# Performance work log

Hardware: AMD Instinct MI355X
Metric: run time of the kernel (lower is better)

The kernel has to match this reference:

```python
import jax, jax.numpy as jnp
import numpy as np

HID, S, SD = 4096, 64, 256
EPS = 1e-5
SCALE = SD ** -0.5


def layer_norm(x, w, b):
    mu = jnp.mean(x, axis=-1, keepdims=True)
    var = jnp.mean(jnp.square(x - mu), axis=-1, keepdims=True)
    return (x - mu) * jax.lax.rsqrt(var + EPS) * w + b


def setup_inputs() -> dict:
    key = jax.random.key(0)
    ks = jax.random.split(key, 9)
    B, T = 4, 4096
    w = lambda k, i, o: jax.random.normal(k, (i, o), jnp.float32) * 0.02
    return {
        "segment_hidden": jax.random.normal(ks[0], (B, T, HID), jnp.float32),
        "slot_embeddings": jax.random.normal(ks[1], (S, HID), jnp.float32) * 0.02,
        "Wq": w(ks[2], HID, SD),
        "Wk": w(ks[3], HID, SD),
        "Wv": w(ks[4], HID, SD),
        "Wo": w(ks[5], SD, HID),
        "Wrq": w(ks[6], HID, SD),
        "Wro": w(ks[7], SD, HID),
        "gate_bias": jnp.full((S,), 2.0, jnp.float32),
        "slot_norm_w": jnp.ones((HID,), jnp.float32),
        "slot_norm_b": jnp.zeros((HID,), jnp.float32),
        "recon_norm_w": jnp.ones((HID,), jnp.float32),
        "recon_norm_b": jnp.zeros((HID,), jnp.float32),
    }


def reference(segment_hidden, slot_embeddings, Wq, Wk, Wv, Wo, Wrq, Wro,
              gate_bias, slot_norm_w, slot_norm_b, recon_norm_w, recon_norm_b):
    B = segment_hidden.shape[0]
    slots = jnp.broadcast_to(slot_embeddings[None], (B, S, HID))

    # 1) slot attention: slots attend to segment
    q = slots @ Wq                      # [B,S,sd]
    k = segment_hidden @ Wk             # [B,T,sd]
    v = segment_hidden @ Wv             # [B,T,sd]
    attn = jax.nn.softmax(jnp.einsum('bsd,btd->bst', q, k) * SCALE, axis=-1)
    out = jnp.einsum('bst,btd->bsd', attn, v) @ Wo
    updated_slots = layer_norm(slots + out, slot_norm_w, slot_norm_b)  # [B,S,D]

    # 2) reconstruction: segment attends to updated slots
    rq = segment_hidden @ Wrq           # [B,T,sd]
    rk = updated_slots @ Wk             # [B,S,sd]
    rv = updated_slots @ Wv             # [B,S,sd]
    rattn = jax.nn.softmax(jnp.einsum('btd,bsd->bts', rq, rk) * SCALE, axis=-1)
    rout = jnp.einsum('bts,bsd->btd', rattn, rv) @ Wro
    rout = layer_norm(rout, recon_norm_w, recon_norm_b)
    scalar_gate = jax.nn.sigmoid(jnp.mean(gate_bias))[None, None, None]  # [1,1,1]
    reconstruction = scalar_gate * rout

    # 3) MSE reconstruction loss
    recon_loss = jnp.mean(jnp.square(reconstruction - segment_hidden))
    return updated_slots, recon_loss, scalar_gate
```

## Files before the change

kernel.cpp:

```cpp
#include <hip/hip_runtime.h>
#include <hip/hip_bf16.h>


#define DEVI __device__ __forceinline__

typedef __attribute__((ext_vector_type(4))) float f32x4;
typedef __attribute__((ext_vector_type(8))) __bf16 bf16x8;

DEVI float bf2f(unsigned short u) {
    unsigned int x = ((unsigned int)u) << 16;
    return __uint_as_float(x);
}
DEVI unsigned short f2bf(float f) {
    unsigned int u = __float_as_uint(f);
    unsigned int r = (u + 0x7FFFu + ((u >> 16) & 1u)) >> 16;
    return (unsigned short)r;
}

DEVI void gl_lds16(const void* g, void* l) {
    __builtin_amdgcn_global_load_lds(
        (const __attribute__((address_space(1))) void*)g,
        (__attribute__((address_space(3))) void*)l, 16, 0, 0);
}

__global__ __launch_bounds__(256) void k_cvt_bf16(const float* __restrict__ in,
                                                  unsigned short* __restrict__ out,
                                                  long n) {
    long i = ((long)blockIdx.x * blockDim.x + threadIdx.x) * 4;
    long stride = (long)gridDim.x * blockDim.x * 4;
    for (long j = i; j < n; j += stride) {
        float4 v = *(const float4*)(in + j);
        ushort4 o;
        o.x = f2bf(v.x); o.y = f2bf(v.y); o.z = f2bf(v.z); o.w = f2bf(v.w);
        *(ushort4*)(out + j) = o;
    }
}

__global__ __launch_bounds__(256) void k_transpose_f2b(const float* __restrict__ in, int ldin, long long sIn,
                                                       unsigned short* __restrict__ out, int ldout, long long sOut) {
    __shared__ float tile[32][33];
    in += (long long)blockIdx.z * sIn;
    out += (long long)blockIdx.z * sOut;
    int c0 = blockIdx.x * 32, r0 = blockIdx.y * 32;
    int tx = threadIdx.x, ty = threadIdx.y;
#pragma unroll
    for (int i = 0; i < 4; i++)
        tile[ty + i * 8][tx] = in[(size_t)(r0 + ty + i * 8) * ldin + c0 + tx];
    __syncthreads();
#pragma unroll
    for (int i = 0; i < 4; i++)
        out[(size_t)(c0 + ty + i * 8) * ldout + r0 + tx] = f2bf(tile[tx][ty + i * 8]);
}

__global__ __launch_bounds__(256) void k_transpose_b2b(const unsigned short* __restrict__ in, int ldin, long long sIn,
                                                       unsigned short* __restrict__ out, int ldout, long long sOut) {
    __shared__ unsigned short tile[32][33];
    in += (long long)blockIdx.z * sIn;
    out += (long long)blockIdx.z * sOut;
    int c0 = blockIdx.x * 32, r0 = blockIdx.y * 32;
    int tx = threadIdx.x, ty = threadIdx.y;
#pragma unroll
    for (int i = 0; i < 4; i++)
        tile[ty + i * 8][tx] = in[(size_t)(r0 + ty + i * 8) * ldin + c0 + tx];
    __syncthreads();
#pragma unroll
    for (int i = 0; i < 4; i++)
        out[(size_t)(c0 + ty + i * 8) * ldout + r0 + tx] = tile[tx][ty + i * 8];
}

template <int BM, int BN, int WR, int WC, int OMODE>
__global__ __launch_bounds__(256) void k_gemm(const unsigned short* __restrict__ A, int lda, long long sA,
                                              const unsigned short* __restrict__ B, int ldb, long long sB,
                                              void* __restrict__ Cv, int ldc, long long sC,
                                              int K, int ksplit, float alpha) {
    constexpr int NW = WR * WC;
    static_assert(NW == 4, "4 waves");
    __shared__ alignas(1024) unsigned short As[BM * 64];
    __shared__ alignas(1024) unsigned short Bs[BN * 64];
    const int tid = threadIdx.x;
    const int lane = tid & 63;
    const int wv = tid >> 6;
    const int batch = blockIdx.z / ksplit;
    const int ks = blockIdx.z - batch * ksplit;
    const unsigned short* Ab = A + (long long)batch * sA;
    const unsigned short* Bb = B + (long long)batch * sB;
    const int bm0 = blockIdx.x * BM;
    const int bn0 = blockIdx.y * BN;
    const int kchunk = K / ksplit;
    const int kt0 = (ks * kchunk) >> 6;
    const int kt1 = ((ks + 1) * kchunk) >> 6;

    constexpr int WTM = BM / WR, WTN = BN / WC;
    constexpr int FM = WTM / 16, FN = WTN / 16;
    const int wr = wv / WC, wc = wv % WC;

    f32x4 acc[FM][FN] = {};

    constexpr int CA = BM / 8, CB = BN / 8;
    constexpr int PW = (CA + CB) / NW;

    for (int kt = kt0; kt < kt1; ++kt) {
        const int k0 = kt << 6;
#pragma unroll
        for (int i = 0; i < PW; i++) {
            int c = wv * PW + i;
            if (c < CA) {
                int row = bm0 + c * 8 + (lane >> 3);
                gl_lds16(Ab + (size_t)row * lda + k0 + (lane & 7) * 8, (void*)(As + c * 512));
            } else {
                int cc = c - CA;
                int row = bn0 + cc * 8 + (lane >> 3);
                gl_lds16(Bb + (size_t)row * ldb + k0 + (lane & 7) * 8, (void*)(Bs + cc * 512));
            }
        }
        asm volatile("s_waitcnt vmcnt(0)" ::: "memory");
        __syncthreads();
#pragma unroll
        for (int kk = 0; kk < 2; ++kk) {
            const int kof = kk * 32 + (lane >> 4) * 8;
            bf16x8 af[FM], bfr[FN];
#pragma unroll
            for (int m = 0; m < FM; m++)
                af[m] = *(const bf16x8*)(As + (wr * WTM + m * 16 + (lane & 15)) * 64 + kof);
#pragma unroll
            for (int n = 0; n < FN; n++)
                bfr[n] = *(const bf16x8*)(Bs + (wc * WTN + n * 16 + (lane & 15)) * 64 + kof);
#pragma unroll
            for (int m = 0; m < FM; m++)
#pragma unroll
                for (int n = 0; n < FN; n++)
                    acc[m][n] = __builtin_amdgcn_mfma_f32_16x16x32_bf16(af[m], bfr[n], acc[m][n], 0, 0, 0);
        }
        __syncthreads();
    }

    float* Cf = (float*)Cv;
    unsigned short* Cb = (unsigned short*)Cv;
    const long long cbase = (long long)batch * sC;
#pragma unroll
    for (int m = 0; m < FM; m++) {
#pragma unroll
        for (int n = 0; n < FN; n++) {
            int gr0 = bm0 + wr * WTM + m * 16 + (lane >> 4) * 4;
            int gc = bn0 + wc * WTN + n * 16 + (lane & 15);
#pragma unroll
            for (int j = 0; j < 4; j++) {
                float v = alpha * acc[m][n][j];
                long long idx = cbase + (long long)(gr0 + j) * ldc + gc;
                if constexpr (OMODE == 0) Cf[idx] = v;
                else if constexpr (OMODE == 1) Cb[idx] = f2bf(v);
                else atomicAdd(Cf + idx, v);
            }
        }
    }
}

DEVI float block_sum(float v, float* sh) {
    int lane = threadIdx.x & 63, wv = threadIdx.x >> 6;
#pragma unroll
    for (int o = 32; o > 0; o >>= 1) v += __shfl_xor(v, o);
    __syncthreads();
    if (lane == 0) sh[wv] = v;
    __syncthreads();
    return sh[0] + sh[1] + sh[2] + sh[3];
}

__global__ __launch_bounds__(256) void k_softmax_T(const float* __restrict__ L,
                                                   unsigned short* __restrict__ out) {
    const size_t row = blockIdx.x;
    const float* x = L + row * 4096;
    float v[16];
    float mx = -1e30f;
#pragma unroll
    for (int i = 0; i < 4; i++) {
        float4 t = *(const float4*)(x + threadIdx.x * 4 + i * 1024);
        v[i * 4 + 0] = t.x; v[i * 4 + 1] = t.y; v[i * 4 + 2] = t.z; v[i * 4 + 3] = t.w;
        mx = fmaxf(fmaxf(fmaxf(mx, t.x), fmaxf(t.y, t.z)), t.w);
    }
    int lane = threadIdx.x & 63, wv = threadIdx.x >> 6;
#pragma unroll
    for (int o = 32; o > 0; o >>= 1) mx = fmaxf(mx, __shfl_xor(mx, o));
    __shared__ float smax[4], ssum[4];
    if (lane == 0) smax[wv] = mx;
    __syncthreads();
    mx = fmaxf(fmaxf(smax[0], smax[1]), fmaxf(smax[2], smax[3]));
    float sum = 0.f;
#pragma unroll
    for (int i = 0; i < 16; i++) {
        v[i] = __expf(v[i] - mx);
        sum += v[i];
    }
#pragma unroll
    for (int o = 32; o > 0; o >>= 1) sum += __shfl_xor(sum, o);
    if (lane == 0) ssum[wv] = sum;
    __syncthreads();
    float inv = 1.0f / (ssum[0] + ssum[1] + ssum[2] + ssum[3]);
    unsigned short* o = out + row * 4096;
#pragma unroll
    for (int i = 0; i < 4; i++) {
        ushort4 u;
        u.x = f2bf(v[i * 4 + 0] * inv); u.y = f2bf(v[i * 4 + 1] * inv);
        u.z = f2bf(v[i * 4 + 2] * inv); u.w = f2bf(v[i * 4 + 3] * inv);
        *(ushort4*)(o + threadIdx.x * 4 + i * 1024) = u;
    }
}

__global__ __launch_bounds__(256) void k_softmax_S(const float* __restrict__ L,
                                                   unsigned short* __restrict__ out) {
    size_t row = (size_t)blockIdx.x * 4 + (threadIdx.x >> 6);
    int lane = threadIdx.x & 63;
    float v = L[row * 64 + lane];
    float mx = v;
#pragma unroll
    for (int o = 32; o > 0; o >>= 1) mx = fmaxf(mx, __shfl_xor(mx, o));
    float e = __expf(v - mx), sum = e;
#pragma unroll
    for (int o = 32; o > 0; o >>= 1) sum += __shfl_xor(sum, o);
    out[row * 64 + lane] = f2bf(e / sum);
}

__global__ __launch_bounds__(256) void k_ln_slots(const float* __restrict__ slot_emb,
                                                  const float* __restrict__ out2,
                                                  const float* __restrict__ w,
                                                  const float* __restrict__ b,
                                                  float* __restrict__ us_out,
                                                  unsigned short* __restrict__ us_b) {
    __shared__ float sh[4];
    int row = blockIdx.x;
    int s = row & 63;
    const float* se_r = slot_emb + (size_t)s * 4096;
    const float* o2_r = out2 + (size_t)row * 4096;
    float x[16];
    float sum = 0.f;
#pragma unroll
    for (int i = 0; i < 4; i++) {
        int j0 = threadIdx.x * 4 + i * 1024;
        float4 a = *(const float4*)(se_r + j0);
        float4 c = *(const float4*)(o2_r + j0);
        x[i * 4 + 0] = a.x + c.x; x[i * 4 + 1] = a.y + c.y;
        x[i * 4 + 2] = a.z + c.z; x[i * 4 + 3] = a.w + c.w;
        sum += x[i * 4 + 0] + x[i * 4 + 1] + x[i * 4 + 2] + x[i * 4 + 3];
    }
    sum = block_sum(sum, sh);
    float mu = sum * (1.0f / 4096.0f);
    float s2 = 0.f;
#pragma unroll
    for (int i = 0; i < 16; i++) {
        float d = x[i] - mu;
        s2 += d * d;
    }
    s2 = block_sum(s2, sh);
    float rs = rsqrtf(s2 * (1.0f / 4096.0f) + 1e-5f);
#pragma unroll
    for (int i = 0; i < 4; i++) {
        int j0 = threadIdx.x * 4 + i * 1024;
        float4 wv4 = *(const float4*)(w + j0);
        float4 bv4 = *(const float4*)(b + j0);
        float4 y;
        y.x = (x[i * 4 + 0] - mu) * rs * wv4.x + bv4.x;
        y.y = (x[i * 4 + 1] - mu) * rs * wv4.y + bv4.y;
        y.z = (x[i * 4 + 2] - mu) * rs * wv4.z + bv4.z;
        y.w = (x[i * 4 + 3] - mu) * rs * wv4.w + bv4.w;
        *(float4*)(us_out + (size_t)row * 4096 + j0) = y;
        ushort4 u;
        u.x = f2bf(y.x); u.y = f2bf(y.y); u.z = f2bf(y.z); u.w = f2bf(y.w);
        *(ushort4*)(us_b + (size_t)row * 4096 + j0) = u;
    }
}

__global__ __launch_bounds__(256) void k_ln_loss(const unsigned short* __restrict__ rout_pre,
                                                 const float* __restrict__ seg,
                                                 const float* __restrict__ w,
                                                 const float* __restrict__ b,
                                                 const float* __restrict__ gate_s,
                                                 float* __restrict__ partials) {
    __shared__ float sh[4];
    size_t row = blockIdx.x;
    const unsigned short* xr = rout_pre + row * 4096;
    const float* sr = seg + row * 4096;
    float x[16];
    float sum = 0.f;
#pragma unroll
    for (int i = 0; i < 4; i++) {
        int j0 = threadIdx.x * 4 + i * 1024;
        ushort4 u = *(const ushort4*)(xr + j0);
        x[i * 4 + 0] = bf2f(u.x); x[i * 4 + 1] = bf2f(u.y);
        x[i * 4 + 2] = bf2f(u.z); x[i * 4 + 3] = bf2f(u.w);
        sum += x[i * 4 + 0] + x[i * 4 + 1] + x[i * 4 + 2] + x[i * 4 + 3];
    }
    sum = block_sum(sum, sh);
    float mu = sum * (1.0f / 4096.0f);
    float s2 = 0.f;
#pragma unroll
    for (int i = 0; i < 16; i++) {
        float d = x[i] - mu;
        s2 += d * d;
    }
    s2 = block_sum(s2, sh);
    float rs = rsqrtf(s2 * (1.0f / 4096.0f) + 1e-5f);
    float g = *gate_s;
    float ls = 0.f;
#pragma unroll
    for (int i = 0; i < 4; i++) {
        int j0 = threadIdx.x * 4 + i * 1024;
        float4 wv4 = *(const float4*)(w + j0);
        float4 bv4 = *(const float4*)(b + j0);
        float4 sv4 = *(const float4*)(sr + j0);
        float d0 = g * ((x[i * 4 + 0] - mu) * rs * wv4.x + bv4.x) - sv4.x;
        float d1 = g * ((x[i * 4 + 1] - mu) * rs * wv4.y + bv4.y) - sv4.y;
        float d2 = g * ((x[i * 4 + 2] - mu) * rs * wv4.z + bv4.z) - sv4.z;
        float d3 = g * ((x[i * 4 + 3] - mu) * rs * wv4.w + bv4.w) - sv4.w;
        ls += d0 * d0 + d1 * d1 + d2 * d2 + d3 * d3;
    }
    ls = block_sum(ls, sh);
    if (threadIdx.x == 0) partials[row] = ls;
}

__global__ void k_gate(const float* __restrict__ gb, float* __restrict__ gate_s) {
    int lane = threadIdx.x;
    float v = gb[lane];
#pragma unroll
    for (int o = 32; o > 0; o >>= 1) v += __shfl_xor(v, o);
    if (lane == 0) *gate_s = 1.0f / (1.0f + __expf(-(v * (1.0f / 64.0f))));
}

__global__ __launch_bounds__(1024) void k_loss_final(const float* __restrict__ partials,
                                                     const float* __restrict__ gate_s,
                                                     float* __restrict__ out) {
    __shared__ float sh[16];
    int t = threadIdx.x;
    float s = 0.f;
#pragma unroll
    for (int i = 0; i < 4; i++) {
        float4 v = *(const float4*)(partials + t * 16 + i * 4);
        s += v.x + v.y + v.z + v.w;
    }
#pragma unroll
    for (int o = 32; o > 0; o >>= 1) s += __shfl_xor(s, o);
    int lane = t & 63, wv = t >> 6;
    if (lane == 0) sh[wv] = s;
    __syncthreads();
    if (t == 0) {
        float tot = 0.f;
#pragma unroll
        for (int i = 0; i < 16; i++) tot += sh[i];
        out[1048576] = tot * (1.0f / 67108864.0f);
        out[1048577] = *gate_s;
    }
}

extern "C" void kernel_launch(void* const* d_in, const int* in_sizes, int n_in,
                              void* d_out, int out_size, void* d_ws, size_t ws_size,
                              hipStream_t stream) {
    const float* seg = (const float*)d_in[0];
    const float* se  = (const float*)d_in[1];
    const float* Wq  = (const float*)d_in[2];
    const float* Wk  = (const float*)d_in[3];
    const float* Wv  = (const float*)d_in[4];
    const float* Wo  = (const float*)d_in[5];
    const float* Wrq = (const float*)d_in[6];
    const float* Wro = (const float*)d_in[7];
    const float* gb  = (const float*)d_in[8];
    const float* snw = (const float*)d_in[9];
    const float* snb = (const float*)d_in[10];
    const float* rnw = (const float*)d_in[11];
    const float* rnb = (const float*)d_in[12];
    float* out = (float*)d_out;

    char* ws = (char*)d_ws;
    size_t off = 0;
    auto alloc = [&](size_t bytes) -> char* {
        char* p = ws + off;
        off += (bytes + 1023) & ~(size_t)1023;
        return p;
    };

    unsigned short* Xb    = (unsigned short*)alloc((size_t)16384 * 4096 * 2);
    unsigned short* KVQ   = (unsigned short*)alloc((size_t)16384 * 768 * 2);
    unsigned short* Wt    = (unsigned short*)alloc((size_t)1024 * 4096 * 2);
    unsigned short* Wot   = (unsigned short*)alloc((size_t)4096 * 256 * 2);
    unsigned short* Wrot  = (unsigned short*)alloc((size_t)4096 * 256 * 2);
    unsigned short* seb   = (unsigned short*)alloc((size_t)64 * 4096 * 2);
    float*          qf    = (float*)alloc((size_t)64 * 256 * 4);
    unsigned short* qb    = (unsigned short*)alloc((size_t)64 * 256 * 2);
    float*          L1    = (float*)alloc((size_t)4 * 64 * 4096 * 4);
    unsigned short* attn  = (unsigned short*)alloc((size_t)4 * 64 * 4096 * 2);
    unsigned short* Vt    = (unsigned short*)alloc((size_t)4 * 256 * 4096 * 2);
    float*          out1f = (float*)alloc((size_t)4 * 64 * 256 * 4);
    unsigned short* out1b = (unsigned short*)alloc((size_t)4 * 64 * 256 * 2);
    float*          out2  = (float*)alloc((size_t)256 * 4096 * 4);
    unsigned short* usb   = (unsigned short*)alloc((size_t)256 * 4096 * 2);
    float*          rkvf  = (float*)alloc((size_t)256 * 512 * 4);
    unsigned short* rkvb  = (unsigned short*)alloc((size_t)256 * 512 * 2);
    unsigned short* rvt   = (unsigned short*)alloc((size_t)4 * 256 * 64 * 2);
    unsigned short* rattn = (unsigned short*)alloc((size_t)4 * 4096 * 64 * 2);
    float*          gate_s = (float*)alloc(64);
    float*          partials = (float*)alloc((size_t)16384 * 4);
    unsigned short* routp = Xb;
    float*          L2    = L1;
    unsigned short* rmid  = Vt;

    hipMemsetAsync(out1f, 0, (size_t)4 * 64 * 256 * 4, stream);
    hipMemsetAsync(rkvf, 0, (size_t)256 * 512 * 4, stream);
    hipMemsetAsync(qf, 0, (size_t)64 * 256 * 4, stream);

    dim3 tb(32, 8);
    k_transpose_f2b<<<dim3(8, 128, 1), tb, 0, stream>>>(Wk, 256, 0, Wt, 4096, 0);
    k_transpose_f2b<<<dim3(8, 128, 1), tb, 0, stream>>>(Wv, 256, 0, Wt + (size_t)256 * 4096, 4096, 0);
    k_transpose_f2b<<<dim3(8, 128, 1), tb, 0, stream>>>(Wrq, 256, 0, Wt + (size_t)512 * 4096, 4096, 0);
    k_transpose_f2b<<<dim3(8, 128, 1), tb, 0, stream>>>(Wq, 256, 0, Wt + (size_t)768 * 4096, 4096, 0);
    k_transpose_f2b<<<dim3(128, 8, 1), tb, 0, stream>>>(Wo, 4096, 0, Wot, 256, 0);
    k_transpose_f2b<<<dim3(128, 8, 1), tb, 0, stream>>>(Wro, 4096, 0, Wrot, 256, 0);

    k_cvt_bf16<<<4096, 256, 0, stream>>>(seg, Xb, (long)67108864);
    k_cvt_bf16<<<256, 256, 0, stream>>>(se, seb, (long)262144);
    k_gate<<<1, 64, 0, stream>>>(gb, gate_s);

    k_gemm<64, 128, 1, 4, 2><<<dim3(1, 2, 16), 256, 0, stream>>>(
        seb, 4096, 0, Wt + (size_t)768 * 4096, 4096, 0, qf, 256, 0, 4096, 16, 1.0f);
    k_cvt_bf16<<<16, 256, 0, stream>>>(qf, qb, (long)16384);

    k_gemm<128, 128, 2, 2, 1><<<dim3(128, 6, 1), 256, 0, stream>>>(
        Xb, 4096, 0, Wt, 4096, 0, KVQ, 768, 0, 4096, 1, 1.0f);

    k_gemm<64, 128, 1, 4, 0><<<dim3(1, 32, 4), 256, 0, stream>>>(
        qb, 256, 0, KVQ, 768, 4096LL * 768, L1, 4096, 64LL * 4096, 256, 1, 0.0625f);
    k_softmax_T<<<256, 256, 0, stream>>>(L1, attn);

    k_transpose_b2b<<<dim3(8, 128, 4), tb, 0, stream>>>(KVQ + 256, 768, 4096LL * 768, Vt, 4096, 256LL * 4096);

    k_gemm<64, 128, 1, 4, 2><<<dim3(1, 2, 64), 256, 0, stream>>>(
        attn, 4096, 64LL * 4096, Vt, 4096, 256LL * 4096, out1f, 256, 64LL * 256, 4096, 16, 1.0f);
    k_cvt_bf16<<<64, 256, 0, stream>>>(out1f, out1b, (long)65536);

    k_gemm<64, 128, 1, 4, 0><<<dim3(4, 32, 1), 256, 0, stream>>>(
        out1b, 256, 0, Wot, 256, 0, out2, 4096, 0, 256, 1, 1.0f);

    k_ln_slots<<<256, 256, 0, stream>>>(se, out2, snw, snb, out, usb);

    k_gemm<64, 128, 1, 4, 2><<<dim3(4, 4, 16), 256, 0, stream>>>(
        usb, 4096, 0, Wt, 4096, 0, rkvf, 512, 0, 4096, 16, 1.0f);
    k_cvt_bf16<<<128, 256, 0, stream>>>(rkvf, rkvb, (long)131072);

    k_transpose_b2b<<<dim3(8, 2, 4), tb, 0, stream>>>(rkvb + 256, 512, 64LL * 512, rvt, 64, 256LL * 64);

    k_gemm<128, 64, 4, 1, 0><<<dim3(32, 1, 4), 256, 0, stream>>>(
        KVQ + 512, 768, 4096LL * 768, L2  == nullptr ? nullptr : rkvb, 512, 64LL * 512, L2, 64, 4096LL * 64, 256, 1, 0.0625f);
    k_softmax_S<<<4096, 256, 0, stream>>>(L2, rattn);

    k_gemm<128, 64, 4, 1, 1><<<dim3(32, 4, 4), 256, 0, stream>>>(
        rattn, 64, 4096LL * 64, rvt, 64, 256LL * 64, rmid, 256, 4096LL * 256, 64, 1, 1.0f);

    k_gemm<128, 128, 2, 2, 1><<<dim3(128, 32, 1), 256, 0, stream>>>(
        rmid, 256, 0, Wrot, 256, 0, routp, 4096, 0, 256, 1, 1.0f);

    k_ln_loss<<<16384, 256, 0, stream>>>(routp, seg, rnw, rnb, gate_s, partials);
    k_loss_final<<<1, 1024, 0, stream>>>(partials, gate_s, out);

    (void)in_sizes; (void)n_in; (void)out_size; (void)ws_size;
}
```

Before: 897.9 us.

## Double-buffer GEMM LDS loads, swizzle LDS layout, remap blocks, vectorize transpose

The GEMM kernel now uses two LDS buffers per operand and prefetches the next K tile with global_load_lds while the current tile runs through MFMA. Partial vmcnt waits and raw s_barrier replace the full waits, which lets memory latency overlap with compute. LDS addresses are XOR-swizzled on the source side to cut bank conflicts on fragment reads, and an optional blockIdx.x remap changes how M tiles are spread across the grid. The bf16 transpose moves to 64x64 tiles with 16-byte vector loads and stores. Together these double LDS use per block, which may lower occupancy.

```diff
diff --git a/kernel.cpp b/kernel.cpp
--- a/kernel.cpp
+++ b/kernel.cpp
@@ -6,6 +6,7 @@
 
 typedef __attribute__((ext_vector_type(4))) float f32x4;
 typedef __attribute__((ext_vector_type(8))) __bf16 bf16x8;
+typedef __attribute__((ext_vector_type(8))) unsigned short u16x8;
 
 DEVI float bf2f(unsigned short u) {
     unsigned int x = ((unsigned int)u) << 16;
@@ -54,37 +55,46 @@
 
 __global__ __launch_bounds__(256) void k_transpose_b2b(const unsigned short* __restrict__ in, int ldin, long long sIn,
                                                        unsigned short* __restrict__ out, int ldout, long long sOut) {
-    __shared__ unsigned short tile[32][33];
+    __shared__ unsigned short tile[64][72];
     in += (long long)blockIdx.z * sIn;
     out += (long long)blockIdx.z * sOut;
-    int c0 = blockIdx.x * 32, r0 = blockIdx.y * 32;
-    int tx = threadIdx.x, ty = threadIdx.y;
-#pragma unroll
-    for (int i = 0; i < 4; i++)
-        tile[ty + i * 8][tx] = in[(size_t)(r0 + ty + i * 8) * ldin + c0 + tx];
-    __syncthreads();
-#pragma unroll
-    for (int i = 0; i < 4; i++)
-        out[(size_t)(c0 + ty + i * 8) * ldout + r0 + tx] = tile[tx][ty + i * 8];
-}
-
-template <int BM, int BN, int WR, int WC, int OMODE>
+    int c0 = blockIdx.x * 64, r0 = blockIdx.y * 64;
+    int t = threadIdx.x;
+    int r = t >> 2, cc = (t & 3) * 16;
+    u16x8 v0 = *(const u16x8*)(in + (size_t)(r0 + r) * ldin + c0 + cc);
+    u16x8 v1 = *(const u16x8*)(in + (size_t)(r0 + r) * ldin + c0 + cc + 8);
+    *(u16x8*)(&tile[r][cc]) = v0;
+    *(u16x8*)(&tile[r][cc + 8]) = v1;
+    __syncthreads();
+    int c = t >> 2, rr = (t & 3) * 16;
+    u16x8 w0, w1;
+#pragma unroll
+    for (int j = 0; j < 8; j++) w0[j] = tile[rr + j][c];
+#pragma unroll
+    for (int j = 0; j < 8; j++) w1[j] = tile[rr + 8 + j][c];
+    *(u16x8*)(out + (size_t)(c0 + c) * ldout + r0 + rr) = w0;
+    *(u16x8*)(out + (size_t)(c0 + c) * ldout + r0 + rr + 8) = w1;
+}
+
+template <int BM, int BN, int WR, int WC, int OMODE, int XSWZ>
 __global__ __launch_bounds__(256) void k_gemm(const unsigned short* __restrict__ A, int lda, long long sA,
                                               const unsigned short* __restrict__ B, int ldb, long long sB,
                                               void* __restrict__ Cv, int ldc, long long sC,
                                               int K, int ksplit, float alpha) {
     constexpr int NW = WR * WC;
     static_assert(NW == 4, "4 waves");
-    __shared__ alignas(1024) unsigned short As[BM * 64];
-    __shared__ alignas(1024) unsigned short Bs[BN * 64];
+    __shared__ alignas(1024) unsigned short As[2][BM * 64];
+    __shared__ alignas(1024) unsigned short Bs[2][BN * 64];
     const int tid = threadIdx.x;
     const int lane = tid & 63;
     const int wv = tid >> 6;
+    int bx = blockIdx.x;
+    if (XSWZ) bx = (bx & 7) * ((int)gridDim.x >> 3) + (bx >> 3);
     const int batch = blockIdx.z / ksplit;
     const int ks = blockIdx.z - batch * ksplit;
     const unsigned short* Ab = A + (long long)batch * sA;
     const unsigned short* Bb = B + (long long)batch * sB;
-    const int bm0 = blockIdx.x * BM;
+    const int bm0 = bx * BM;
     const int bn0 = blockIdx.y * BN;
     const int kchunk = K / ksplit;
     const int kt0 = (ks * kchunk) >> 6;
@@ -99,39 +109,73 @@
     constexpr int CA = BM / 8, CB = BN / 8;
     constexpr int PW = (CA + CB) / NW;
 
-    for (int kt = kt0; kt < kt1; ++kt) {
+    const int srcswz = 8 * ((lane & 7) ^ (lane >> 3));
+    const int rlane = lane >> 3;
+
+    int aof[2][FM], bof[2][FN];
+#pragma unroll
+    for (int kk = 0; kk < 2; kk++) {
+        const int kofs = kk * 32 + (lane >> 4) * 8;
+#pragma unroll
+        for (int m = 0; m < FM; m++) {
+            int r = wr * WTM + m * 16 + (lane & 15);
+            aof[kk][m] = r * 64 + (kofs ^ ((r & 7) << 3));
+        }
+#pragma unroll
+        for (int n = 0; n < FN; n++) {
+            int r = wc * WTN + n * 16 + (lane & 15);
+            bof[kk][n] = r * 64 + (kofs ^ ((r & 7) << 3));
+        }
+    }
+
+    auto stage = [&](int buf, int kt) {
         const int k0 = kt << 6;
 #pragma unroll
         for (int i = 0; i < PW; i++) {
             int c = wv * PW + i;
             if (c < CA) {
-                int row = bm0 + c * 8 + (lane >> 3);
-                gl_lds16(Ab + (size_t)row * lda + k0 + (lane & 7) * 8, (void*)(As + c * 512));
+                int row = bm0 + c * 8 + rlane;
+                gl_lds16(Ab + (size_t)row * lda + k0 + srcswz, (void*)(As[buf] + c * 512));
             } else {
                 int cc = c - CA;
-                int row = bn0 + cc * 8 + (lane >> 3);
-                gl_lds16(Bb + (size_t)row * ldb + k0 + (lane & 7) * 8, (void*)(Bs + cc * 512));
+                int row = bn0 + cc * 8 + rlane;
+                gl_lds16(Bb + (size_t)row * ldb + k0 + srcswz, (void*)(Bs[buf] + cc * 512));
             }
         }
-        asm volatile("s_waitcnt vmcnt(0)" ::: "memory");
-        __syncthreads();
+    };
+
+    stage(0, kt0);
+    int cur = 0;
+    for (int kt = kt0; kt < kt1; ++kt) {
+        const bool hasnext = (kt + 1 < kt1);
+        if (hasnext) {
+            stage(cur ^ 1, kt + 1);
+            if constexpr (PW == 8) asm volatile("s_waitcnt vmcnt(8)" ::: "memory");
+            else if constexpr (PW == 6) asm volatile("s_waitcnt vmcnt(6)" ::: "memory");
+            else asm volatile("s_waitcnt vmcnt(0)" ::: "memory");
+        } else {
+            asm volatile("s_waitcnt vmcnt(0)" ::: "memory");
+        }
+        __builtin_amdgcn_s_barrier();
+        asm volatile("" ::: "memory");
+        const unsigned short* Ac = As[cur];
+        const unsigned short* Bc = Bs[cur];
 #pragma unroll
         for (int kk = 0; kk < 2; ++kk) {
-            const int kof = kk * 32 + (lane >> 4) * 8;
             bf16x8 af[FM], bfr[FN];
 #pragma unroll
-            for (int m = 0; m < FM; m++)
-                af[m] = *(const bf16x8*)(As + (wr * WTM + m * 16 + (lane & 15)) * 64 + kof);
-#pragma unroll
-            for (int n = 0; n < FN; n++)
-                bfr[n] = *(const bf16x8*)(Bs + (wc * WTN + n * 16 + (lane & 15)) * 64 + kof);
+            for (int m = 0; m < FM; m++) af[m] = *(const bf16x8*)(Ac + aof[kk][m]);
+#pragma unroll
+            for (int n = 0; n < FN; n++) bfr[n] = *(const bf16x8*)(Bc + bof[kk][n]);
 #pragma unroll
             for (int m = 0; m < FM; m++)
 #pragma unroll
                 for (int n = 0; n < FN; n++)
                     acc[m][n] = __builtin_amdgcn_mfma_f32_16x16x32_bf16(af[m], bfr[n], acc[m][n], 0, 0, 0);
         }
-        __syncthreads();
+        asm volatile("" ::: "memory");
+        __builtin_amdgcn_s_barrier();
+        cur ^= 1;
     }
 
     float* Cf = (float*)Cv;
@@ -416,42 +460,42 @@
     k_cvt_bf16<<<256, 256, 0, stream>>>(se, seb, (long)262144);
     k_gate<<<1, 64, 0, stream>>>(gb, gate_s);
 
-    k_gemm<64, 128, 1, 4, 2><<<dim3(1, 2, 16), 256, 0, stream>>>(
+    k_gemm<64, 128, 1, 4, 2, 0><<<dim3(1, 2, 16), 256, 0, stream>>>(
         seb, 4096, 0, Wt + (size_t)768 * 4096, 4096, 0, qf, 256, 0, 4096, 16, 1.0f);
     k_cvt_bf16<<<16, 256, 0, stream>>>(qf, qb, (long)16384);
 
-    k_gemm<128, 128, 2, 2, 1><<<dim3(128, 6, 1), 256, 0, stream>>>(
+    k_gemm<128, 128, 2, 2, 1, 1><<<dim3(128, 6, 1), 256, 0, stream>>>(
         Xb, 4096, 0, Wt, 4096, 0, KVQ, 768, 0, 4096, 1, 1.0f);
 
-    k_gemm<64, 128, 1, 4, 0><<<dim3(1, 32, 4), 256, 0, stream>>>(
+    k_gemm<64, 128, 1, 4, 0, 0><<<dim3(1, 32, 4), 256, 0, stream>>>(
         qb, 256, 0, KVQ, 768, 4096LL * 768, L1, 4096, 64LL * 4096, 256, 1, 0.0625f);
     k_softmax_T<<<256, 256, 0, stream>>>(L1, attn);
 
-    k_transpose_b2b<<<dim3(8, 128, 4), tb, 0, stream>>>(KVQ + 256, 768, 4096LL * 768, Vt, 4096, 256LL * 4096);
-
-    k_gemm<64, 128, 1, 4, 2><<<dim3(1, 2, 64), 256, 0, stream>>>(
+    k_transpose_b2b<<<dim3(4, 64, 4), 256, 0, stream>>>(KVQ + 256, 768, 4096LL * 768, Vt, 4096, 256LL * 4096);
+
+    k_gemm<64, 128, 1, 4, 2, 0><<<dim3(1, 2, 64), 256, 0, stream>>>(
         attn, 4096, 64LL * 4096, Vt, 4096, 256LL * 4096, out1f, 256, 64LL * 256, 4096, 16, 1.0f);
     k_cvt_bf16<<<64, 256, 0, stream>>>(out1f, out1b, (long)65536);
 
-    k_gemm<64, 128, 1, 4, 0><<<dim3(4, 32, 1), 256, 0, stream>>>(
+    k_gemm<64, 128, 1, 4, 0, 0><<<dim3(4, 32, 1), 256, 0, stream>>>(
         out1b, 256, 0, Wot, 256, 0, out2, 4096, 0, 256, 1, 1.0f);
 
     k_ln_slots<<<256, 256, 0, stream>>>(se, out2, snw, snb, out, usb);
 
-    k_gemm<64, 128, 1, 4, 2><<<dim3(4, 4, 16), 256, 0, stream>>>(
+    k_gemm<64, 128, 1, 4, 2, 0><<<dim3(4, 4, 16), 256, 0, stream>>>(
         usb, 4096, 0, Wt, 4096, 0, rkvf, 512, 0, 4096, 16, 1.0f);
     k_cvt_bf16<<<128, 256, 0, stream>>>(rkvf, rkvb, (long)131072);
 
-    k_transpose_b2b<<<dim3(8, 2, 4), tb, 0, stream>>>(rkvb + 256, 512, 64LL * 512, rvt, 64, 256LL * 64);
-
-    k_gemm<128, 64, 4, 1, 0><<<dim3(32, 1, 4), 256, 0, stream>>>(
-        KVQ + 512, 768, 4096LL * 768, L2  == nullptr ? nullptr : rkvb, 512, 64LL * 512, L2, 64, 4096LL * 64, 256, 1, 0.0625f);
+    k_transpose_b2b<<<dim3(4, 1, 4), 256, 0, stream>>>(rkvb + 256, 512, 64LL * 512, rvt, 64, 256LL * 64);
+
+    k_gemm<128, 64, 4, 1, 0, 1><<<dim3(32, 1, 4), 256, 0, stream>>>(
+        KVQ + 512, 768, 4096LL * 768, rkvb, 512, 64LL * 512, L2, 64, 4096LL * 64, 256, 1, 0.0625f);
     k_softmax_S<<<4096, 256, 0, stream>>>(L2, rattn);
 
-    k_gemm<128, 64, 4, 1, 1><<<dim3(32, 4, 4), 256, 0, stream>>>(
+    k_gemm<128, 64, 4, 1, 1, 1><<<dim3(32, 4, 4), 256, 0, stream>>>(
         rattn, 64, 4096LL * 64, rvt, 64, 256LL * 64, rmid, 256, 4096LL * 256, 64, 1, 1.0f);
 
-    k_gemm<128, 128, 2, 2, 1><<<dim3(128, 32, 1), 256, 0, stream>>>(
+    k_gemm<128, 128, 2, 2, 1, 1><<<dim3(128, 32, 1), 256, 0, stream>>>(
         rmid, 256, 0, Wrot, 256, 0, routp, 4096, 0, 256, 1, 1.0f);
 
     k_ln_loss<<<16384, 256, 0, stream>>>(routp, seg, rnw, rnb, gate_s, partials);
```

Result: faster. 785.5 us (-12.5%).
